# Performance work log

Measured on AMD Instinct MI355X. Metric: run time of the kernel, lower is better.

## Reference

```python
import jax, jax.numpy as jnp
import numpy as np

N_NODES = 50000
N_EDGES = 800000
D_FEAT = 64
HIDDEN = 64
OUT = 2


def setup_inputs() -> dict:
    key = jax.random.key(0)
    ks = jax.random.split(key, 12)
    s = 1.0 / np.sqrt(D_FEAT)
    h = 1.0 / np.sqrt(HIDDEN)
    return {
        "x": jax.random.normal(ks[0], (N_NODES, D_FEAT), jnp.float32),
        "edge_index": jax.random.randint(ks[1], (2, N_EDGES), 0, N_NODES, jnp.int64),
        # SAGEConv layer 1: lin_l (aggregated neighbors, with bias), lin_r (root, no bias)
        "W1l": jax.random.uniform(ks[2], (D_FEAT, HIDDEN), jnp.float32, -s, s),
        "b1": jnp.zeros((HIDDEN,), jnp.float32),
        "W1r": jax.random.uniform(ks[3], (D_FEAT, HIDDEN), jnp.float32, -s, s),
        # SAGEConv layer 2
        "W2l": jax.random.uniform(ks[4], (HIDDEN, HIDDEN), jnp.float32, -h, h),
        "b2": jnp.zeros((HIDDEN,), jnp.float32),
        "W2r": jax.random.uniform(ks[5], (HIDDEN, HIDDEN), jnp.float32, -h, h),
        # final Linear
        "Wlin": jax.random.uniform(ks[6], (HIDDEN, OUT), jnp.float32, -h, h),
        "blin": jnp.zeros((OUT,), jnp.float32),
    }


def _sage_conv(h, src, dst, n_nodes, Wl, bl, Wr):
    # mean-aggregate source features at target nodes (PyG SAGEConv, aggr='mean')
    msgs = h[src]  # [E, d] gather
    agg = jax.ops.segment_sum(msgs, dst, num_segments=n_nodes)
    cnt = jax.ops.segment_sum(jnp.ones((src.shape[0],), h.dtype), dst, num_segments=n_nodes)
    agg = agg / jnp.maximum(cnt, 1.0)[:, None]
    return agg @ Wl + bl + h @ Wr


def reference(x, edge_index, W1l, b1, W1r, W2l, b2, W2r, Wlin, blin):
    src, dst = edge_index[0], edge_index[1]
    n = x.shape[0]
    h1 = jax.nn.relu(_sage_conv(x, src, dst, n, W1l, b1, W1r))
    h2 = jax.nn.relu(_sage_conv(h1, src, dst, n, W2l, b2, W2r))
    return h2 @ Wlin + blin
```

## Files before the change

kernel.cpp:

```cpp
#include <hip/hip_runtime.h>
#include <hip/hip_fp16.h>

namespace {

constexpr int N = 50000;
constexpr int E = 800000;
constexpr int D = 64;
constexpr int TN = 128;
constexpr int APAD = 132;
constexpr int CAP = 64;
constexpr int NR = 256;
constexpr int RW = 196;
constexpr int CAPR = 3584;
constexpr int EPB = 2048;

using floatx2 = __attribute__((ext_vector_type(2))) float;

__device__ __forceinline__ uint2 pack4h(float a, float b, float c, float d) {
  __half2 lo = __floats2half2_rn(a, b);
  __half2 hi = __floats2half2_rn(c, d);
  uint2 u;
  u.x = *reinterpret_cast<unsigned*>(&lo);
  u.y = *reinterpret_cast<unsigned*>(&hi);
  return u;
}

__device__ __forceinline__ unsigned pack4fp8(float a, float b, float c, float d) {
  int u = __builtin_amdgcn_cvt_pk_fp8_f32(a, b, 0, false);
  u = __builtin_amdgcn_cvt_pk_fp8_f32(c, d, u, true);
  return (unsigned)u;
}
__device__ __forceinline__ void acc4fp8(unsigned u, float* a) {
  floatx2 lo = __builtin_amdgcn_cvt_pk_f32_fp8((int)u, false);
  floatx2 hi = __builtin_amdgcn_cvt_pk_f32_fp8((int)u, true);
  a[0] += lo[0]; a[1] += lo[1]; a[2] += hi[0]; a[3] += hi[1];
}

__device__ __forceinline__ void gemm_core(float (*a_s)[APAD],
                                          const float* __restrict__ Wl,
                                          const float* __restrict__ Wr,
                                          const float* __restrict__ bias,
                                          unsigned* __restrict__ P,
                                          __half* __restrict__ Q, int n, int base) {
  int tid = threadIdx.x;
  int ng = tid & 15;
  int cg = tid >> 4;

  float acc[8][8];
#pragma unroll
  for (int i = 0; i < 8; ++i)
#pragma unroll
    for (int j = 0; j < 8; ++j) acc[i][j] = (j < 4) ? 0.0f : bias[cg * 4 + (j - 4)];

#pragma unroll 4
  for (int k = 0; k < D; ++k) {
    float4 a0 = *(const float4*)&a_s[k][ng * 4];
    float4 a1 = *(const float4*)&a_s[k][64 + ng * 4];
    float4 w0 = *(const float4*)&Wl[k * D + cg * 4];
    float4 w1 = *(const float4*)&Wr[k * D + cg * 4];
    float av[8] = {a0.x, a0.y, a0.z, a0.w, a1.x, a1.y, a1.z, a1.w};
    float wv[8] = {w0.x, w0.y, w0.z, w0.w, w1.x, w1.y, w1.z, w1.w};
#pragma unroll
    for (int i = 0; i < 8; ++i)
#pragma unroll
      for (int j = 0; j < 8; ++j) acc[i][j] = fmaf(av[i], wv[j], acc[i][j]);
  }

  uint2* Qv = (uint2*)Q;
#pragma unroll
  for (int i = 0; i < 8; ++i) {
    int gn = base + ((i < 4) ? (ng * 4 + i) : (64 + ng * 4 + (i - 4)));
    if (gn < n) {
      P[(size_t)gn * 16 + cg] = pack4fp8(acc[i][0], acc[i][1], acc[i][2], acc[i][3]);
      Qv[(size_t)gn * 16 + cg] = pack4h(acc[i][4], acc[i][5], acc[i][6], acc[i][7]);
    }
  }
}

__device__ __forceinline__ void stage_a_f32(float (*a_s)[APAD],
                                            const float* __restrict__ A, int n, int base) {
  int tid = threadIdx.x;
  const float4* A4 = (const float4*)A;
  for (int i = tid; i < TN * 16; i += 256) {
    int node = i & 127;
    int kq = i >> 7;
    int gn = base + node;
    float4 v = (gn < n) ? A4[(size_t)gn * 16 + kq] : make_float4(0.f, 0.f, 0.f, 0.f);
    a_s[kq * 4 + 0][node] = v.x;
    a_s[kq * 4 + 1][node] = v.y;
    a_s[kq * 4 + 2][node] = v.z;
    a_s[kq * 4 + 3][node] = v.w;
  }
  __syncthreads();
}

__device__ __forceinline__ void stage_a_f16(float (*a_s)[APAD],
                                            const __half* __restrict__ A, int n, int base) {
  int tid = threadIdx.x;
  const uint2* A2 = (const uint2*)A;
  for (int i = tid; i < TN * 16; i += 256) {
    int node = i & 127;
    int kq = i >> 7;
    int gn = base + node;
    uint2 u;
    u.x = 0u; u.y = 0u;
    if (gn < n) u = A2[(size_t)gn * 16 + kq];
    float2 fa = __half22float2(*reinterpret_cast<const __half2*>(&u.x));
    float2 fb = __half22float2(*reinterpret_cast<const __half2*>(&u.y));
    a_s[kq * 4 + 0][node] = fa.x;
    a_s[kq * 4 + 1][node] = fa.y;
    a_s[kq * 4 + 2][node] = fb.x;
    a_s[kq * 4 + 3][node] = fb.y;
  }
  __syncthreads();
}

__device__ __forceinline__ void place_phase1(const int* __restrict__ src,
                                             const int* __restrict__ dst,
                                             int* __restrict__ cursor,
                                             unsigned int* __restrict__ staging,
                                             int nE, int blk) {
  __shared__ int hist[NR];
  __shared__ int hist2[NR];
  __shared__ int rbase[NR];
  int t = threadIdx.x;
  for (int i = t; i < NR; i += 256) { hist[i] = 0; hist2[i] = 0; }
  __syncthreads();

  int e0 = blk * EPB + t * 8;
  int rr[8];
  unsigned dlo[8];
#pragma unroll
  for (int j = 0; j < 8; ++j) {
    int e = e0 + j;
    if (e < nE) {
      unsigned d = (unsigned)dst[e];
      unsigned r = d / RW;
      rr[j] = (int)r;
      dlo[j] = d - r * RW;
      atomicAdd(&hist[r], 1);
    } else {
      rr[j] = -1;
    }
  }
  __syncthreads();
  if (t < NR) rbase[t] = hist[t] ? atomicAdd(&cursor[t], hist[t]) : 0;
  __syncthreads();
#pragma unroll
  for (int j = 0; j < 8; ++j) {
    if (rr[j] >= 0) {
      unsigned s = (unsigned)src[e0 + j];
      int q = atomicAdd(&hist2[rr[j]], 1);
      int off = rbase[rr[j]] + q;
      if (off < CAPR)
        staging[(size_t)rr[j] * CAPR + off] = (s << 8) | dlo[j];
    }
  }
}

__global__ __launch_bounds__(256) void gemm_place_kernel(
    const float* __restrict__ A, const float* __restrict__ Wl,
    const float* __restrict__ Wr, const float* __restrict__ bias,
    unsigned* __restrict__ P, __half* __restrict__ Q, int n, int nGB,
    const int* __restrict__ src, const int* __restrict__ dst,
    int* __restrict__ cursor, unsigned int* __restrict__ staging, int nE) {
  __shared__ float a_s[D][APAD];
  if ((int)blockIdx.x < nGB) {
    stage_a_f32(a_s, A, n, blockIdx.x * TN);
    gemm_core(a_s, Wl, Wr, bias, P, Q, n, blockIdx.x * TN);
  } else {
    place_phase1(src, dst, cursor, staging, nE, (int)blockIdx.x - nGB);
  }
}

__global__ __launch_bounds__(1024) void place_phase2(
    const unsigned int* __restrict__ staging, const int* __restrict__ cursor,
    unsigned short* __restrict__ bucket, int* __restrict__ cntg) {
  __shared__ int lcnt[RW];
  int t = threadIdx.x;
  int r = blockIdx.x;
  for (int i = t; i < RW; i += 1024) lcnt[i] = 0;
  __syncthreads();

  int M = min(cursor[r], CAPR);
  const unsigned int* st = staging + (size_t)r * CAPR;
  int nbase = r * RW;
  for (int i = t; i < M; i += 1024) {
    unsigned v = st[i];
    int nl = (int)(v & 255u);
    unsigned s = v >> 8;
    int p = atomicAdd(&lcnt[nl], 1);
    if (p < CAP) bucket[(size_t)(nbase + nl) * CAP + p] = (unsigned short)s;
  }
  __syncthreads();
  for (int i = t; i < RW; i += 1024) {
    int node = nbase + i;
    if (node < N) cntg[node] = lcnt[i];
  }
}

__global__ __launch_bounds__(256) void gemm2_kernel(const __half* __restrict__ A,
                                                    const float* __restrict__ Wl,
                                                    const float* __restrict__ Wr,
                                                    const float* __restrict__ bias,
                                                    unsigned* __restrict__ P,
                                                    __half* __restrict__ Q, int n) {
  __shared__ float a_s[D][APAD];
  stage_a_f16(a_s, A, n, blockIdx.x * TN);
  gemm_core(a_s, Wl, Wr, bias, P, Q, n, blockIdx.x * TN);
}

__device__ __forceinline__ void gather_pair(const uint2* __restrict__ Pv2,
                                            const uint2* __restrict__ Qv,
                                            const unsigned short* __restrict__ bucket,
                                            const int* __restrict__ cntg,
                                            int n0, int n1, int r8, int c8,
                                            float* h0, float* h1) {
  int ct0 = cntg[n0];
  int ct1 = cntg[n1];
  uint2 q00 = Qv[(size_t)n0 * 16 + c8 * 2 + 0];
  uint2 q01 = Qv[(size_t)n0 * 16 + c8 * 2 + 1];
  uint2 q10 = Qv[(size_t)n1 * 16 + c8 * 2 + 0];
  uint2 q11 = Qv[(size_t)n1 * 16 + c8 * 2 + 1];

  float sc0 = 1.0f / fmaxf((float)ct0, 1.0f);
  float sc1 = 1.0f / fmaxf((float)ct1, 1.0f);
  int c0 = min(ct0, CAP);
  int c1 = min(ct1, CAP);
  const unsigned short* sl0 = bucket + (size_t)n0 * CAP;
  const unsigned short* sl1 = bucket + (size_t)n1 * CAP;

  float a0[8], a1[8];
#pragma unroll
  for (int j = 0; j < 8; ++j) { a0[j] = 0.0f; a1[j] = 0.0f; }

  int cmax = max(c0, c1);
  for (int i0 = r8; i0 < cmax; i0 += 32) {
    int cm0 = max(c0 - 1, 0);
    int cm1 = max(c1 - 1, 0);
    int s00 = sl0[min(i0, cm0)];
    int s01 = sl0[min(i0 + 8, cm0)];
    int s02 = sl0[min(i0 + 16, cm0)];
    int s03 = sl0[min(i0 + 24, cm0)];
    int s10 = sl1[min(i0, cm1)];
    int s11 = sl1[min(i0 + 8, cm1)];
    int s12 = sl1[min(i0 + 16, cm1)];
    int s13 = sl1[min(i0 + 24, cm1)];
    uint2 z; z.x = 0u; z.y = 0u;
    uint2 u00 = z, u01 = z, u02 = z, u03 = z;
    uint2 u10 = z, u11 = z, u12 = z, u13 = z;
    if (i0 < c0)      u00 = Pv2[(size_t)s00 * 8 + c8];
    if (i0 + 8 < c0)  u01 = Pv2[(size_t)s01 * 8 + c8];
    if (i0 + 16 < c0) u02 = Pv2[(size_t)s02 * 8 + c8];
    if (i0 + 24 < c0) u03 = Pv2[(size_t)s03 * 8 + c8];
    if (i0 < c1)      u10 = Pv2[(size_t)s10 * 8 + c8];
    if (i0 + 8 < c1)  u11 = Pv2[(size_t)s11 * 8 + c8];
    if (i0 + 16 < c1) u12 = Pv2[(size_t)s12 * 8 + c8];
    if (i0 + 24 < c1) u13 = Pv2[(size_t)s13 * 8 + c8];
    acc4fp8(u00.x, a0); acc4fp8(u00.y, a0 + 4);
    acc4fp8(u01.x, a0); acc4fp8(u01.y, a0 + 4);
    acc4fp8(u02.x, a0); acc4fp8(u02.y, a0 + 4);
    acc4fp8(u03.x, a0); acc4fp8(u03.y, a0 + 4);
    acc4fp8(u10.x, a1); acc4fp8(u10.y, a1 + 4);
    acc4fp8(u11.x, a1); acc4fp8(u11.y, a1 + 4);
    acc4fp8(u12.x, a1); acc4fp8(u12.y, a1 + 4);
    acc4fp8(u13.x, a1); acc4fp8(u13.y, a1 + 4);
  }
#pragma unroll
  for (int j = 0; j < 8; ++j) {
    a0[j] += __shfl_xor(a0[j], 8, 64);
    a0[j] += __shfl_xor(a0[j], 16, 64);
    a0[j] += __shfl_xor(a0[j], 32, 64);
    a1[j] += __shfl_xor(a1[j], 8, 64);
    a1[j] += __shfl_xor(a1[j], 16, 64);
    a1[j] += __shfl_xor(a1[j], 32, 64);
  }

  float2 qa, qb;
  qa = __half22float2(*reinterpret_cast<const __half2*>(&q00.x));
  qb = __half22float2(*reinterpret_cast<const __half2*>(&q00.y));
  float q0v[8];
  q0v[0] = qa.x; q0v[1] = qa.y; q0v[2] = qb.x; q0v[3] = qb.y;
  qa = __half22float2(*reinterpret_cast<const __half2*>(&q01.x));
  qb = __half22float2(*reinterpret_cast<const __half2*>(&q01.y));
  q0v[4] = qa.x; q0v[5] = qa.y; q0v[6] = qb.x; q0v[7] = qb.y;
  float q1v[8];
  qa = __half22float2(*reinterpret_cast<const __half2*>(&q10.x));
  qb = __half22float2(*reinterpret_cast<const __half2*>(&q10.y));
  q1v[0] = qa.x; q1v[1] = qa.y; q1v[2] = qb.x; q1v[3] = qb.y;
  qa = __half22float2(*reinterpret_cast<const __half2*>(&q11.x));
  qb = __half22float2(*reinterpret_cast<const __half2*>(&q11.y));
  q1v[4] = qa.x; q1v[5] = qa.y; q1v[6] = qb.x; q1v[7] = qb.y;

#pragma unroll
  for (int j = 0; j < 8; ++j) {
    h0[j] = fmaxf(fmaf(a0[j], sc0, q0v[j]), 0.0f);
    h1[j] = fmaxf(fmaf(a1[j], sc1, q1v[j]), 0.0f);
  }
}

__global__ __launch_bounds__(256, 5) void gather1_kernel(
    const unsigned* __restrict__ P, const __half* __restrict__ Q,
    const unsigned short* __restrict__ bucket, const int* __restrict__ cntg,
    __half* __restrict__ hout, int n) {
  int tid = threadIdx.x;
  int lane = tid & 63;
  int sub = tid >> 6;
  int n0 = blockIdx.x * 8 + sub * 2;
  int n1 = n0 + 1;
  if (n1 >= n) {
    if (n0 >= n) return;
    n1 = n0;
  }

  int r8 = lane >> 3;
  int c8 = lane & 7;
  float h0[8], h1[8];
  gather_pair((const uint2*)P, (const uint2*)Q, bucket, cntg, n0, n1, r8, c8, h0, h1);

  if (r8 < 2) {
    const float* h = (r8 == 0) ? h0 : h1;
    int node = (r8 == 0) ? n0 : n1;
    uint4 u;
    uint2 lo = pack4h(h[0], h[1], h[2], h[3]);
    uint2 hi = pack4h(h[4], h[5], h[6], h[7]);
    u.x = lo.x; u.y = lo.y; u.z = hi.x; u.w = hi.y;
    ((uint4*)hout)[(size_t)node * 8 + c8] = u;
  }
}

__global__ __launch_bounds__(256, 5) void gather_final_kernel(
    const unsigned* __restrict__ P, const __half* __restrict__ Q,
    const unsigned short* __restrict__ bucket, const int* __restrict__ cntg,
    const float* __restrict__ Wlin, const float* __restrict__ blin,
    float* __restrict__ outp, int n) {
  int tid = threadIdx.x;
  int lane = tid & 63;
  int sub = tid >> 6;
  int n0 = blockIdx.x * 8 + sub * 2;
  int n1 = n0 + 1;
  if (n1 >= n) {
    if (n0 >= n) return;
    n1 = n0;
  }

  int r8 = lane >> 3;
  int c8 = lane & 7;
  float h0[8], h1[8];
  gather_pair((const uint2*)P, (const uint2*)Q, bucket, cntg, n0, n1, r8, c8, h0, h1);

  const float2* W2 = (const float2*)Wlin;
  float a00 = 0.f, a01 = 0.f, a10 = 0.f, a11 = 0.f;
#pragma unroll
  for (int j = 0; j < 8; ++j) {
    float2 w = W2[c8 * 8 + j];
    a00 = fmaf(h0[j], w.x, a00);
    a01 = fmaf(h0[j], w.y, a01);
    a10 = fmaf(h1[j], w.x, a10);
    a11 = fmaf(h1[j], w.y, a11);
  }
#pragma unroll
  for (int ofs = 4; ofs > 0; ofs >>= 1) {
    a00 += __shfl_xor(a00, ofs, 64);
    a01 += __shfl_xor(a01, ofs, 64);
    a10 += __shfl_xor(a10, ofs, 64);
    a11 += __shfl_xor(a11, ofs, 64);
  }
  if (lane == 0) {
    outp[(size_t)n0 * 2 + 0] = a00 + blin[0];
    outp[(size_t)n0 * 2 + 1] = a01 + blin[1];
  }
  if (lane == 8 && n1 != n0) {
    outp[(size_t)n1 * 2 + 0] = a10 + blin[0];
    outp[(size_t)n1 * 2 + 1] = a11 + blin[1];
  }
}

}

extern "C" void kernel_launch(void* const* d_in, const int* in_sizes, int n_in,
                              void* d_out, int out_size, void* d_ws, size_t ws_size,
                              hipStream_t stream) {
  const float* x    = (const float*)d_in[0];
  const int*   ei   = (const int*)d_in[1];
  const float* W1l  = (const float*)d_in[2];
  const float* b1   = (const float*)d_in[3];
  const float* W1r  = (const float*)d_in[4];
  const float* W2l  = (const float*)d_in[5];
  const float* b2   = (const float*)d_in[6];
  const float* W2r  = (const float*)d_in[7];
  const float* Wlin = (const float*)d_in[8];
  const float* blin = (const float*)d_in[9];
  float* out = (float*)d_out;

  char* ws = (char*)d_ws;
  size_t p = 0;
  unsigned*       P1   = (unsigned*)(ws + p);       p += (size_t)N * D;
  __half*         Q1   = (__half*)(ws + p);         p += (size_t)N * D * 2;
  __half*         hh   = (__half*)(ws + p);         p += (size_t)N * D * 2;
  unsigned*       P2   = (unsigned*)(ws + p);       p += (size_t)N * D;
  __half*         Q2   = (__half*)(ws + p);         p += (size_t)N * D * 2;
  unsigned short* bkt  = (unsigned short*)(ws + p); p += (size_t)N * CAP * 2;
  int*            cntg = (int*)(ws + p);            p += (size_t)((N * 4 + 255) & ~255);
  unsigned int*   stg  = (unsigned int*)(ws + p);   p += (size_t)NR * CAPR * 4;
  int*            cur  = (int*)(ws + p);            p += (size_t)NR * 4;

  const int* src = ei;
  const int* dst = ei + E;

  const int GB = (N + TN - 1) / TN;
  const int PB = (E + EPB - 1) / EPB;

  hipMemsetAsync(cur, 0, (size_t)NR * sizeof(int), stream);

  gemm_place_kernel<<<GB + PB, 256, 0, stream>>>(
      x, W1l, W1r, b1, P1, Q1, N, GB, src, dst, cur, stg, E);

  place_phase2<<<NR, 1024, 0, stream>>>(stg, cur, bkt, cntg);

  gather1_kernel<<<(N + 7) / 8, 256, 0, stream>>>(P1, Q1, bkt, cntg, hh, N);

  gemm2_kernel<<<GB, 256, 0, stream>>>(hh, W2l, W2r, b2, P2, Q2, N);

  gather_final_kernel<<<(N + 7) / 8, 256, 0, stream>>>(
      P2, Q2, bkt, cntg, Wlin, blin, out, N);
}
```

Before: 107.2 us.

## Fuse layer-1 gather with layer-2 GEMM through shared memory

Merges the layer-1 mean-aggregation gather and the layer-2 dense transform into one kernel. Each block gathers 32 nodes' hidden features into LDS, then each thread computes 8 output columns of P2/Q2 for one node, reading weights straight from global/cache. This removes the fp16 intermediate hidden buffer round trip and one kernel launch. In exchange the GEMM no longer uses the tiled staged-weight core, so per-thread weight loads and FMA work may be less efficient, and occupancy drops to 4 blocks.

```diff
diff --git a/kernel.cpp b/kernel.cpp
--- a/kernel.cpp
+++ b/kernel.cpp
@@ -94,27 +94,6 @@
   __syncthreads();
 }
 
-__device__ __forceinline__ void stage_a_f16(float (*a_s)[APAD],
-                                            const __half* __restrict__ A, int n, int base) {
-  int tid = threadIdx.x;
-  const uint2* A2 = (const uint2*)A;
-  for (int i = tid; i < TN * 16; i += 256) {
-    int node = i & 127;
-    int kq = i >> 7;
-    int gn = base + node;
-    uint2 u;
-    u.x = 0u; u.y = 0u;
-    if (gn < n) u = A2[(size_t)gn * 16 + kq];
-    float2 fa = __half22float2(*reinterpret_cast<const __half2*>(&u.x));
-    float2 fb = __half22float2(*reinterpret_cast<const __half2*>(&u.y));
-    a_s[kq * 4 + 0][node] = fa.x;
-    a_s[kq * 4 + 1][node] = fa.y;
-    a_s[kq * 4 + 2][node] = fb.x;
-    a_s[kq * 4 + 3][node] = fb.y;
-  }
-  __syncthreads();
-}
-
 __device__ __forceinline__ void place_phase1(const int* __restrict__ src,
                                              const int* __restrict__ dst,
                                              int* __restrict__ cursor,
@@ -197,17 +176,6 @@
     int node = nbase + i;
     if (node < N) cntg[node] = lcnt[i];
   }
-}
-
-__global__ __launch_bounds__(256) void gemm2_kernel(const __half* __restrict__ A,
-                                                    const float* __restrict__ Wl,
-                                                    const float* __restrict__ Wr,
-                                                    const float* __restrict__ bias,
-                                                    unsigned* __restrict__ P,
-                                                    __half* __restrict__ Q, int n) {
-  __shared__ float a_s[D][APAD];
-  stage_a_f16(a_s, A, n, blockIdx.x * TN);
-  gemm_core(a_s, Wl, Wr, bias, P, Q, n, blockIdx.x * TN);
 }
 
 __device__ __forceinline__ void gather_pair(const uint2* __restrict__ Pv2,
@@ -299,33 +267,67 @@
   }
 }
 
-__global__ __launch_bounds__(256, 5) void gather1_kernel(
-    const unsigned* __restrict__ P, const __half* __restrict__ Q,
+__global__ __launch_bounds__(256, 4) void layer2_kernel(
+    const unsigned* __restrict__ P1, const __half* __restrict__ Q1,
     const unsigned short* __restrict__ bucket, const int* __restrict__ cntg,
-    __half* __restrict__ hout, int n) {
+    const float* __restrict__ W2l, const float* __restrict__ W2r,
+    const float* __restrict__ b2,
+    unsigned* __restrict__ P2, __half* __restrict__ Q2, int n) {
+  __shared__ float h_lds[32][68];
   int tid = threadIdx.x;
   int lane = tid & 63;
-  int sub = tid >> 6;
-  int n0 = blockIdx.x * 8 + sub * 2;
-  int n1 = n0 + 1;
-  if (n1 >= n) {
-    if (n0 >= n) return;
-    n1 = n0;
-  }
-
+  int wave = tid >> 6;
+  int base = blockIdx.x * 32;
   int r8 = lane >> 3;
   int c8 = lane & 7;
-  float h0[8], h1[8];
-  gather_pair((const uint2*)P, (const uint2*)Q, bucket, cntg, n0, n1, r8, c8, h0, h1);
-
-  if (r8 < 2) {
-    const float* h = (r8 == 0) ? h0 : h1;
-    int node = (r8 == 0) ? n0 : n1;
-    uint4 u;
-    uint2 lo = pack4h(h[0], h[1], h[2], h[3]);
-    uint2 hi = pack4h(h[4], h[5], h[6], h[7]);
-    u.x = lo.x; u.y = lo.y; u.z = hi.x; u.w = hi.y;
-    ((uint4*)hout)[(size_t)node * 8 + c8] = u;
+
+#pragma unroll
+  for (int it = 0; it < 4; ++it) {
+    int l0 = wave * 8 + it * 2;
+    int n0 = min(base + l0, n - 1);
+    int n1 = min(base + l0 + 1, n - 1);
+    float h0[8], h1[8];
+    gather_pair((const uint2*)P1, (const uint2*)Q1, bucket, cntg, n0, n1, r8, c8, h0, h1);
+    if (r8 == 0) {
+#pragma unroll
+      for (int j = 0; j < 8; ++j) h_lds[l0][c8 * 8 + j] = h0[j];
+    } else if (r8 == 1) {
+#pragma unroll
+      for (int j = 0; j < 8; ++j) h_lds[l0 + 1][c8 * 8 + j] = h1[j];
+    }
+  }
+  __syncthreads();
+
+  int m = tid >> 3;
+  int s = tid & 7;
+  int gn = base + m;
+  float accp[8], accq[8];
+#pragma unroll
+  for (int j = 0; j < 8; ++j) { accp[j] = 0.0f; accq[j] = b2[s * 8 + j]; }
+  const float4* Wl4 = (const float4*)W2l;
+  const float4* Wr4 = (const float4*)W2r;
+#pragma unroll 4
+  for (int k = 0; k < D; ++k) {
+    float hk = h_lds[m][k];
+    float4 wl0 = Wl4[k * 16 + s * 2 + 0];
+    float4 wl1 = Wl4[k * 16 + s * 2 + 1];
+    float4 wr0 = Wr4[k * 16 + s * 2 + 0];
+    float4 wr1 = Wr4[k * 16 + s * 2 + 1];
+    accp[0] = fmaf(hk, wl0.x, accp[0]); accp[1] = fmaf(hk, wl0.y, accp[1]);
+    accp[2] = fmaf(hk, wl0.z, accp[2]); accp[3] = fmaf(hk, wl0.w, accp[3]);
+    accp[4] = fmaf(hk, wl1.x, accp[4]); accp[5] = fmaf(hk, wl1.y, accp[5]);
+    accp[6] = fmaf(hk, wl1.z, accp[6]); accp[7] = fmaf(hk, wl1.w, accp[7]);
+    accq[0] = fmaf(hk, wr0.x, accq[0]); accq[1] = fmaf(hk, wr0.y, accq[1]);
+    accq[2] = fmaf(hk, wr0.z, accq[2]); accq[3] = fmaf(hk, wr0.w, accq[3]);
+    accq[4] = fmaf(hk, wr1.x, accq[4]); accq[5] = fmaf(hk, wr1.y, accq[5]);
+    accq[6] = fmaf(hk, wr1.z, accq[6]); accq[7] = fmaf(hk, wr1.w, accq[7]);
+  }
+  if (gn < n) {
+    P2[(size_t)gn * 16 + s * 2 + 0] = pack4fp8(accp[0], accp[1], accp[2], accp[3]);
+    P2[(size_t)gn * 16 + s * 2 + 1] = pack4fp8(accp[4], accp[5], accp[6], accp[7]);
+    uint2* Qv = (uint2*)Q2;
+    Qv[(size_t)gn * 16 + s * 2 + 0] = pack4h(accq[0], accq[1], accq[2], accq[3]);
+    Qv[(size_t)gn * 16 + s * 2 + 1] = pack4h(accq[4], accq[5], accq[6], accq[7]);
   }
 }
 
@@ -397,7 +399,6 @@
   size_t p = 0;
   unsigned*       P1   = (unsigned*)(ws + p);       p += (size_t)N * D;
   __half*         Q1   = (__half*)(ws + p);         p += (size_t)N * D * 2;
-  __half*         hh   = (__half*)(ws + p);         p += (size_t)N * D * 2;
   unsigned*       P2   = (unsigned*)(ws + p);       p += (size_t)N * D;
   __half*         Q2   = (__half*)(ws + p);         p += (size_t)N * D * 2;
   unsigned short* bkt  = (unsigned short*)(ws + p); p += (size_t)N * CAP * 2;
@@ -418,9 +419,8 @@
 
   place_phase2<<<NR, 1024, 0, stream>>>(stg, cur, bkt, cntg);
 
-  gather1_kernel<<<(N + 7) / 8, 256, 0, stream>>>(P1, Q1, bkt, cntg, hh, N);
-
-  gemm2_kernel<<<GB, 256, 0, stream>>>(hh, W2l, W2r, b2, P2, Q2, N);
+  layer2_kernel<<<(N + 31) / 32, 256, 0, stream>>>(
+      P1, Q1, bkt, cntg, W2l, W2r, b2, P2, Q2, N);
 
   gather_final_kernel<<<(N + 7) / 8, 256, 0, stream>>>(
       P2, Q2, bkt, cntg, Wlin, blin, out, N);
```

After: 134.5 us. +25.4%, slower.

## Fuse layer-2 GEMM into final gather with aggregate-then-transform on FP8 features

Applied to the files above, without the earlier changes.

Removes the separate layer-2 GEMM kernel and its P2/Q2 intermediates. The final kernel now gathers neighbor features of h1 (stored additionally as FP8 by the layer-1 gather), takes their mean, then applies W2l/W2r, bias, ReLU and the output linear in registers with shuffles. This drops one launch and one full pass over node features, at the cost of per-node matvec work in the gather kernel and reduced precision in the neighbor aggregation.

```diff
diff --git a/kernel.cpp b/kernel.cpp
--- a/kernel.cpp
+++ b/kernel.cpp
@@ -94,27 +94,6 @@
   __syncthreads();
 }
 
-__device__ __forceinline__ void stage_a_f16(float (*a_s)[APAD],
-                                            const __half* __restrict__ A, int n, int base) {
-  int tid = threadIdx.x;
-  const uint2* A2 = (const uint2*)A;
-  for (int i = tid; i < TN * 16; i += 256) {
-    int node = i & 127;
-    int kq = i >> 7;
-    int gn = base + node;
-    uint2 u;
-    u.x = 0u; u.y = 0u;
-    if (gn < n) u = A2[(size_t)gn * 16 + kq];
-    float2 fa = __half22float2(*reinterpret_cast<const __half2*>(&u.x));
-    float2 fb = __half22float2(*reinterpret_cast<const __half2*>(&u.y));
-    a_s[kq * 4 + 0][node] = fa.x;
-    a_s[kq * 4 + 1][node] = fa.y;
-    a_s[kq * 4 + 2][node] = fb.x;
-    a_s[kq * 4 + 3][node] = fb.y;
-  }
-  __syncthreads();
-}
-
 __device__ __forceinline__ void place_phase1(const int* __restrict__ src,
                                              const int* __restrict__ dst,
                                              int* __restrict__ cursor,
@@ -197,17 +176,6 @@
     int node = nbase + i;
     if (node < N) cntg[node] = lcnt[i];
   }
-}
-
-__global__ __launch_bounds__(256) void gemm2_kernel(const __half* __restrict__ A,
-                                                    const float* __restrict__ Wl,
-                                                    const float* __restrict__ Wr,
-                                                    const float* __restrict__ bias,
-                                                    unsigned* __restrict__ P,
-                                                    __half* __restrict__ Q, int n) {
-  __shared__ float a_s[D][APAD];
-  stage_a_f16(a_s, A, n, blockIdx.x * TN);
-  gemm_core(a_s, Wl, Wr, bias, P, Q, n, blockIdx.x * TN);
 }
 
 __device__ __forceinline__ void gather_pair(const uint2* __restrict__ Pv2,
@@ -302,7 +270,7 @@
 __global__ __launch_bounds__(256, 5) void gather1_kernel(
     const unsigned* __restrict__ P, const __half* __restrict__ Q,
     const unsigned short* __restrict__ bucket, const int* __restrict__ cntg,
-    __half* __restrict__ hout, int n) {
+    __half* __restrict__ h16, unsigned* __restrict__ h8, int n) {
   int tid = threadIdx.x;
   int lane = tid & 63;
   int sub = tid >> 6;
@@ -325,15 +293,98 @@
     uint2 lo = pack4h(h[0], h[1], h[2], h[3]);
     uint2 hi = pack4h(h[4], h[5], h[6], h[7]);
     u.x = lo.x; u.y = lo.y; u.z = hi.x; u.w = hi.y;
-    ((uint4*)hout)[(size_t)node * 8 + c8] = u;
-  }
-}
-
-__global__ __launch_bounds__(256, 5) void gather_final_kernel(
-    const unsigned* __restrict__ P, const __half* __restrict__ Q,
+    ((uint4*)h16)[(size_t)node * 8 + c8] = u;
+    uint2 u8;
+    u8.x = pack4fp8(h[0], h[1], h[2], h[3]);
+    u8.y = pack4fp8(h[4], h[5], h[6], h[7]);
+    ((uint2*)h8)[(size_t)node * 8 + c8] = u8;
+  }
+}
+
+__device__ __forceinline__ void gather_mean_pair(const uint2* __restrict__ H8,
+                                                 const uint4* __restrict__ H16,
+                                                 const unsigned short* __restrict__ bucket,
+                                                 const int* __restrict__ cntg,
+                                                 int n0, int n1, int r8, int c8,
+                                                 float* agg0, float* agg1,
+                                                 float* self0, float* self1) {
+  int ct0 = cntg[n0];
+  int ct1 = cntg[n1];
+  uint4 s0u = H16[(size_t)n0 * 8 + c8];
+  uint4 s1u = H16[(size_t)n1 * 8 + c8];
+
+  float sc0 = 1.0f / fmaxf((float)ct0, 1.0f);
+  float sc1 = 1.0f / fmaxf((float)ct1, 1.0f);
+  int c0 = min(ct0, CAP);
+  int c1 = min(ct1, CAP);
+  const unsigned short* sl0 = bucket + (size_t)n0 * CAP;
+  const unsigned short* sl1 = bucket + (size_t)n1 * CAP;
+
+  float a0[8], a1[8];
+#pragma unroll
+  for (int j = 0; j < 8; ++j) { a0[j] = 0.0f; a1[j] = 0.0f; }
+
+  int cmax = max(c0, c1);
+  for (int i0 = r8; i0 < cmax; i0 += 32) {
+    int cm0 = max(c0 - 1, 0);
+    int cm1 = max(c1 - 1, 0);
+    int s00 = sl0[min(i0, cm0)];
+    int s01 = sl0[min(i0 + 8, cm0)];
+    int s02 = sl0[min(i0 + 16, cm0)];
+    int s03 = sl0[min(i0 + 24, cm0)];
+    int s10 = sl1[min(i0, cm1)];
+    int s11 = sl1[min(i0 + 8, cm1)];
+    int s12 = sl1[min(i0 + 16, cm1)];
+    int s13 = sl1[min(i0 + 24, cm1)];
+    uint2 z; z.x = 0u; z.y = 0u;
+    uint2 u00 = z, u01 = z, u02 = z, u03 = z;
+    uint2 u10 = z, u11 = z, u12 = z, u13 = z;
+    if (i0 < c0)      u00 = H8[(size_t)s00 * 8 + c8];
+    if (i0 + 8 < c0)  u01 = H8[(size_t)s01 * 8 + c8];
+    if (i0 + 16 < c0) u02 = H8[(size_t)s02 * 8 + c8];
+    if (i0 + 24 < c0) u03 = H8[(size_t)s03 * 8 + c8];
+    if (i0 < c1)      u10 = H8[(size_t)s10 * 8 + c8];
+    if (i0 + 8 < c1)  u11 = H8[(size_t)s11 * 8 + c8];
+    if (i0 + 16 < c1) u12 = H8[(size_t)s12 * 8 + c8];
+    if (i0 + 24 < c1) u13 = H8[(size_t)s13 * 8 + c8];
+    acc4fp8(u00.x, a0); acc4fp8(u00.y, a0 + 4);
+    acc4fp8(u01.x, a0); acc4fp8(u01.y, a0 + 4);
+    acc4fp8(u02.x, a0); acc4fp8(u02.y, a0 + 4);
+    acc4fp8(u03.x, a0); acc4fp8(u03.y, a0 + 4);
+    acc4fp8(u10.x, a1); acc4fp8(u10.y, a1 + 4);
+    acc4fp8(u11.x, a1); acc4fp8(u11.y, a1 + 4);
+    acc4fp8(u12.x, a1); acc4fp8(u12.y, a1 + 4);
+    acc4fp8(u13.x, a1); acc4fp8(u13.y, a1 + 4);
+  }
+#pragma unroll
+  for (int j = 0; j < 8; ++j) {
+    a0[j] += __shfl_xor(a0[j], 8, 64);
+    a0[j] += __shfl_xor(a0[j], 16, 64);
+    a0[j] += __shfl_xor(a0[j], 32, 64);
+    a1[j] += __shfl_xor(a1[j], 8, 64);
+    a1[j] += __shfl_xor(a1[j], 16, 64);
+    a1[j] += __shfl_xor(a1[j], 32, 64);
+  }
+#pragma unroll
+  for (int j = 0; j < 8; ++j) { agg0[j] = a0[j] * sc0; agg1[j] = a1[j] * sc1; }
+
+  float2 f;
+  f = __half22float2(*reinterpret_cast<const __half2*>(&s0u.x)); self0[0] = f.x; self0[1] = f.y;
+  f = __half22float2(*reinterpret_cast<const __half2*>(&s0u.y)); self0[2] = f.x; self0[3] = f.y;
+  f = __half22float2(*reinterpret_cast<const __half2*>(&s0u.z)); self0[4] = f.x; self0[5] = f.y;
+  f = __half22float2(*reinterpret_cast<const __half2*>(&s0u.w)); self0[6] = f.x; self0[7] = f.y;
+  f = __half22float2(*reinterpret_cast<const __half2*>(&s1u.x)); self1[0] = f.x; self1[1] = f.y;
+  f = __half22float2(*reinterpret_cast<const __half2*>(&s1u.y)); self1[2] = f.x; self1[3] = f.y;
+  f = __half22float2(*reinterpret_cast<const __half2*>(&s1u.z)); self1[4] = f.x; self1[5] = f.y;
+  f = __half22float2(*reinterpret_cast<const __half2*>(&s1u.w)); self1[6] = f.x; self1[7] = f.y;
+}
+
+__global__ __launch_bounds__(256, 4) void layer2_final_kernel(
+    const unsigned* __restrict__ H8, const __half* __restrict__ H16,
     const unsigned short* __restrict__ bucket, const int* __restrict__ cntg,
-    const float* __restrict__ Wlin, const float* __restrict__ blin,
-    float* __restrict__ outp, int n) {
+    const float* __restrict__ W2l, const float* __restrict__ W2r,
+    const float* __restrict__ b2, const float* __restrict__ Wlin,
+    const float* __restrict__ blin, float* __restrict__ outp, int n) {
   int tid = threadIdx.x;
   int lane = tid & 63;
   int sub = tid >> 6;
@@ -346,33 +397,81 @@
 
   int r8 = lane >> 3;
   int c8 = lane & 7;
-  float h0[8], h1[8];
-  gather_pair((const uint2*)P, (const uint2*)Q, bucket, cntg, n0, n1, r8, c8, h0, h1);
+  float agg0[8], agg1[8], self0[8], self1[8];
+  gather_mean_pair((const uint2*)H8, (const uint4*)H16, bucket, cntg,
+                   n0, n1, r8, c8, agg0, agg1, self0, self1);
+
+  float z0[8], z1[8];
+#pragma unroll
+  for (int j = 0; j < 8; ++j) { z0[j] = 0.0f; z1[j] = 0.0f; }
+  const float4* Wl4 = (const float4*)W2l;
+  const float4* Wr4 = (const float4*)W2r;
+#pragma unroll
+  for (int kk = 0; kk < 8; ++kk) {
+    int k = c8 * 8 + kk;
+    float4 wl0 = Wl4[k * 16 + r8 * 2 + 0];
+    float4 wl1 = Wl4[k * 16 + r8 * 2 + 1];
+    float4 wr0 = Wr4[k * 16 + r8 * 2 + 0];
+    float4 wr1 = Wr4[k * 16 + r8 * 2 + 1];
+    float a0k = agg0[kk], s0k = self0[kk];
+    float a1k = agg1[kk], s1k = self1[kk];
+    z0[0] = fmaf(a0k, wl0.x, fmaf(s0k, wr0.x, z0[0]));
+    z0[1] = fmaf(a0k, wl0.y, fmaf(s0k, wr0.y, z0[1]));
+    z0[2] = fmaf(a0k, wl0.z, fmaf(s0k, wr0.z, z0[2]));
+    z0[3] = fmaf(a0k, wl0.w, fmaf(s0k, wr0.w, z0[3]));
+    z0[4] = fmaf(a0k, wl1.x, fmaf(s0k, wr1.x, z0[4]));
+    z0[5] = fmaf(a0k, wl1.y, fmaf(s0k, wr1.y, z0[5]));
+    z0[6] = fmaf(a0k, wl1.z, fmaf(s0k, wr1.z, z0[6]));
+    z0[7] = fmaf(a0k, wl1.w, fmaf(s0k, wr1.w, z0[7]));
+    z1[0] = fmaf(a1k, wl0.x, fmaf(s1k, wr0.x, z1[0]));
+    z1[1] = fmaf(a1k, wl0.y, fmaf(s1k, wr0.y, z1[1]));
+    z1[2] = fmaf(a1k, wl0.z, fmaf(s1k, wr0.z, z1[2]));
+    z1[3] = fmaf(a1k, wl0.w, fmaf(s1k, wr0.w, z1[3]));
+    z1[4] = fmaf(a1k, wl1.x, fmaf(s1k, wr1.x, z1[4]));
+    z1[5] = fmaf(a1k, wl1.y, fmaf(s1k, wr1.y, z1[5]));
+    z1[6] = fmaf(a1k, wl1.z, fmaf(s1k, wr1.z, z1[6]));
+    z1[7] = fmaf(a1k, wl1.w, fmaf(s1k, wr1.w, z1[7]));
+  }
+#pragma unroll
+  for (int j = 0; j < 8; ++j) {
+    z0[j] += __shfl_xor(z0[j], 1, 64);
+    z0[j] += __shfl_xor(z0[j], 2, 64);
+    z0[j] += __shfl_xor(z0[j], 4, 64);
+    z1[j] += __shfl_xor(z1[j], 1, 64);
+    z1[j] += __shfl_xor(z1[j], 2, 64);
+    z1[j] += __shfl_xor(z1[j], 4, 64);
+  }
+#pragma unroll
+  for (int j = 0; j < 8; ++j) {
+    float b = b2[r8 * 8 + j];
+    z0[j] = fmaxf(z0[j] + b, 0.0f);
+    z1[j] = fmaxf(z1[j] + b, 0.0f);
+  }
 
   const float2* W2 = (const float2*)Wlin;
-  float a00 = 0.f, a01 = 0.f, a10 = 0.f, a11 = 0.f;
-#pragma unroll
-  for (int j = 0; j < 8; ++j) {
-    float2 w = W2[c8 * 8 + j];
-    a00 = fmaf(h0[j], w.x, a00);
-    a01 = fmaf(h0[j], w.y, a01);
-    a10 = fmaf(h1[j], w.x, a10);
-    a11 = fmaf(h1[j], w.y, a11);
-  }
-#pragma unroll
-  for (int ofs = 4; ofs > 0; ofs >>= 1) {
-    a00 += __shfl_xor(a00, ofs, 64);
-    a01 += __shfl_xor(a01, ofs, 64);
-    a10 += __shfl_xor(a10, ofs, 64);
-    a11 += __shfl_xor(a11, ofs, 64);
+  float o00 = 0.f, o01 = 0.f, o10 = 0.f, o11 = 0.f;
+#pragma unroll
+  for (int j = 0; j < 8; ++j) {
+    float2 w = W2[r8 * 8 + j];
+    o00 = fmaf(z0[j], w.x, o00);
+    o01 = fmaf(z0[j], w.y, o01);
+    o10 = fmaf(z1[j], w.x, o10);
+    o11 = fmaf(z1[j], w.y, o11);
+  }
+#pragma unroll
+  for (int ofs = 8; ofs <= 32; ofs <<= 1) {
+    o00 += __shfl_xor(o00, ofs, 64);
+    o01 += __shfl_xor(o01, ofs, 64);
+    o10 += __shfl_xor(o10, ofs, 64);
+    o11 += __shfl_xor(o11, ofs, 64);
   }
   if (lane == 0) {
-    outp[(size_t)n0 * 2 + 0] = a00 + blin[0];
-    outp[(size_t)n0 * 2 + 1] = a01 + blin[1];
-  }
-  if (lane == 8 && n1 != n0) {
-    outp[(size_t)n1 * 2 + 0] = a10 + blin[0];
-    outp[(size_t)n1 * 2 + 1] = a11 + blin[1];
+    outp[(size_t)n0 * 2 + 0] = o00 + blin[0];
+    outp[(size_t)n0 * 2 + 1] = o01 + blin[1];
+  }
+  if (lane == 1 && n1 != n0) {
+    outp[(size_t)n1 * 2 + 0] = o10 + blin[0];
+    outp[(size_t)n1 * 2 + 1] = o11 + blin[1];
   }
 }
 
@@ -397,9 +496,8 @@
   size_t p = 0;
   unsigned*       P1   = (unsigned*)(ws + p);       p += (size_t)N * D;
   __half*         Q1   = (__half*)(ws + p);         p += (size_t)N * D * 2;
-  __half*         hh   = (__half*)(ws + p);         p += (size_t)N * D * 2;
-  unsigned*       P2   = (unsigned*)(ws + p);       p += (size_t)N * D;
-  __half*         Q2   = (__half*)(ws + p);         p += (size_t)N * D * 2;
+  __half*         h16  = (__half*)(ws + p);         p += (size_t)N * D * 2;
+  unsigned*       h8   = (unsigned*)(ws + p);       p += (size_t)N * D;
   unsigned short* bkt  = (unsigned short*)(ws + p); p += (size_t)N * CAP * 2;
   int*            cntg = (int*)(ws + p);            p += (size_t)((N * 4 + 255) & ~255);
   unsigned int*   stg  = (unsigned int*)(ws + p);   p += (size_t)NR * CAPR * 4;
@@ -418,10 +516,8 @@
 
   place_phase2<<<NR, 1024, 0, stream>>>(stg, cur, bkt, cntg);
 
-  gather1_kernel<<<(N + 7) / 8, 256, 0, stream>>>(P1, Q1, bkt, cntg, hh, N);
-
-  gemm2_kernel<<<GB, 256, 0, stream>>>(hh, W2l, W2r, b2, P2, Q2, N);
-
-  gather_final_kernel<<<(N + 7) / 8, 256, 0, stream>>>(
-      P2, Q2, bkt, cntg, Wlin, blin, out, N);
-}
+  gather1_kernel<<<(N + 7) / 8, 256, 0, stream>>>(P1, Q1, bkt, cntg, h16, h8, N);
+
+  layer2_final_kernel<<<(N + 7) / 8, 256, 0, stream>>>(
+      h8, h16, bkt, cntg, W2l, W2r, b2, Wlin, blin, out, N);
+}
```

Result: slower. 166.1 us (+54.9%).
